# Kernel tuning notes

Measured on AMD Instinct MI355X. Metric: run time of the kernel, lower is better.

Reference implementation:

```python
import jax, jax.numpy as jnp
import numpy as np

NUM_BLOCKS = 4
B, S, D = 4, 4096, 1024
A, FF = 1024, 4096
LN_EPS = 1e-6


def _ln(x, s, b):
    m = jnp.mean(x, axis=-1, keepdims=True)
    v = jnp.mean(jnp.square(x - m), axis=-1, keepdims=True)
    return (x - m) * jax.lax.rsqrt(v + LN_EPS) * s + b


def setup_inputs() -> dict:
    key = jax.random.key(0)
    ks = jax.random.split(key, 8)
    w = lambda k, shape: jax.random.normal(k, shape, dtype=jnp.float32) * 0.02
    return {
        "x": jax.random.normal(ks[0], (B, S, D), dtype=jnp.float32),
        "Wq": w(ks[1], (NUM_BLOCKS, D, A)), "bq": jnp.zeros((NUM_BLOCKS, A), jnp.float32),
        "Wk": w(ks[2], (NUM_BLOCKS, D, A)), "bk": jnp.zeros((NUM_BLOCKS, A), jnp.float32),
        "Wv": w(ks[3], (NUM_BLOCKS, D, A)), "bv": jnp.zeros((NUM_BLOCKS, A), jnp.float32),
        "Wo": w(ks[4], (NUM_BLOCKS, A, D)), "bo": jnp.zeros((NUM_BLOCKS, D), jnp.float32),
        "ln1_s": jnp.ones((NUM_BLOCKS, D), jnp.float32), "ln1_b": jnp.zeros((NUM_BLOCKS, D), jnp.float32),
        "W1": w(ks[5], (NUM_BLOCKS, D, FF)), "b1": jnp.zeros((NUM_BLOCKS, FF), jnp.float32),
        "W2": w(ks[6], (NUM_BLOCKS, FF, D)), "b2": jnp.zeros((NUM_BLOCKS, D), jnp.float32),
        "ln2_s": jnp.ones((NUM_BLOCKS, D), jnp.float32), "ln2_b": jnp.zeros((NUM_BLOCKS, D), jnp.float32),
    }


def reference(x, Wq, bq, Wk, bk, Wv, bv, Wo, bo, ln1_s, ln1_b,
              W1, b1, W2, b2, ln2_s, ln2_b):
    for i in range(NUM_BLOCKS):
        residual = x
        # --- linear attention (elu+1 feature map, elementwise KV aggregation) ---
        q = x @ Wq[i] + bq[i]            # [B,S,A]
        k = x @ Wk[i] + bk[i]
        v = x @ Wv[i] + bv[i]
        Q = jax.nn.elu(q) + 1.0
        K = jax.nn.elu(k) + 1.0
        KV = jnp.einsum('nsh,nsh->nh', K, v, precision='highest')   # [B,A]
        Ksum = jnp.sum(K, axis=1)                                    # [B,A]
        Z = 1.0 / (Q * Ksum[:, None, :] + 1e-6)
        V = Q * KV[:, None, :] * Z                                   # [B,S,A]
        a = jax.nn.gelu(V @ Wo[i] + bo[i])   # gelu inside LinearAttention
        a = jax.nn.gelu(a)                   # gelu in the block body
        x = _ln(a + residual, ln1_s[i], ln1_b[i])
        # --- feedforward ---
        residual = x
        h = jax.nn.gelu(x @ W1[i] + b1[i])
        f = jax.nn.gelu(h @ W2[i] + b2[i])
        x = _ln(f + residual, ln2_s[i], ln2_b[i])
    return x
```

## Files before the change

### kernel.cpp

```cpp
#include <hip/hip_runtime.h>
#include <hip/hip_bf16.h>

typedef unsigned short u16;

#define B_  4
#define S_  4096
#define D_  1024
#define A_  1024
#define FF_ 4096
#define NB  4
#define LN_EPS 1e-6f

typedef __bf16 bf16x8 __attribute__((ext_vector_type(8)));
typedef float  floatx4 __attribute__((ext_vector_type(4)));

__device__ __forceinline__ float gelu_f(float x) {
    float u = 0.7978845608028654f * (x + 0.044715f * x * x * x);
    return x / (1.0f + __expf(-2.0f * u));
}

__device__ __forceinline__ u16 f2bf(float f) {
    __bf16 h = (__bf16)f;
    return *(u16*)&h;
}

__device__ __forceinline__ float bf2f(u16 u) {
    unsigned int v = ((unsigned int)u) << 16;
    float f;
    __builtin_memcpy(&f, &v, 4);
    return f;
}

__device__ __forceinline__ void gload_lds16(const u16* g, u16* l) {
    __builtin_amdgcn_global_load_lds(
        (const __attribute__((address_space(1))) void*)g,
        (__attribute__((address_space(3))) void*)l, 16, 0, 0);
}

__global__ __launch_bounds__(256) void zero_kv(float* __restrict__ p) {
    int idx = (blockIdx.x * 256 + threadIdx.x) * 4;
    *(float4*)(p + idx) = (float4){0.f, 0.f, 0.f, 0.f};
}

__global__ __launch_bounds__(256) void transpose_w(const float* __restrict__ W,
                                                   u16* __restrict__ Wt,
                                                   int K, int N) {
    __shared__ float tile[32][33];
    int tx = threadIdx.x;
    int ty = threadIdx.y;
    int n0 = blockIdx.x * 32;
    int k0 = blockIdx.y * 32;
#pragma unroll
    for (int r = 0; r < 4; r++) {
        int k = k0 + ty + r * 8;
        tile[ty + r * 8][tx] = W[(size_t)k * N + n0 + tx];
    }
    __syncthreads();
#pragma unroll
    for (int r = 0; r < 4; r++) {
        int n = n0 + ty + r * 8;
        Wt[(size_t)n * K + k0 + tx] = f2bf(tile[tx][ty + r * 8]);
    }
}

#define BAR  { asm volatile("" ::: "memory"); __builtin_amdgcn_s_barrier(); \
               asm volatile("" ::: "memory"); }
#define VMC4 asm volatile("s_waitcnt vmcnt(4)" ::: "memory")
#define PRIO1 __builtin_amdgcn_s_setprio(1)
#define PRIO0 __builtin_amdgcn_s_setprio(0)

#define STG(BASE, P, LD, BUF, H, KT) {                                         \
    const u16* s_ = (P) + (size_t)((H) * 128) * (LD) + (KT) * 64;              \
    u16* d_ = (BASE) + (BUF) * 16384 + (H) * 8192 + t * 8;                     \
    gload_lds16(s_, d_);                                                       \
    gload_lds16(s_ + (size_t)64 * (LD), d_ + 4096); }

#define LDA4(BUF, IH) {                                                        \
    _Pragma("unroll") for (int ii = 0; ii < 4; ii++) {                         \
        const u16* p_ = As0 + (BUF) * 16384 + aro + ((IH) * 4 + ii) * 1024;    \
        a[ii][0] = *(const bf16x8*)(p_ + sl0);                                 \
        a[ii][1] = *(const bf16x8*)(p_ + sl1); } }

#define LDB2(BUF, JH) {                                                        \
    _Pragma("unroll") for (int jj = 0; jj < 2; jj++) {                         \
        const u16* p_ = Bs0 + (BUF) * 16384 + bro + ((JH) * 2 + jj) * 1024;    \
        b[(JH) * 2 + jj][0] = *(const bf16x8*)(p_ + sl0);                      \
        b[(JH) * 2 + jj][1] = *(const bf16x8*)(p_ + sl1); } }

#define MM(IH, JH) {                                                           \
    _Pragma("unroll") for (int ii = 0; ii < 4; ii++)                           \
    _Pragma("unroll") for (int jj = 0; jj < 2; jj++)                           \
    _Pragma("unroll") for (int s = 0; s < 2; s++)                              \
        acc[(IH) * 4 + ii][(JH) * 2 + jj] =                                    \
            __builtin_amdgcn_mfma_f32_16x16x32_bf16(                           \
                a[ii][s], b[(JH) * 2 + jj][s],                                 \
                acc[(IH) * 4 + ii][(JH) * 2 + jj], 0, 0, 0); }

template <int MODE>
__global__ __launch_bounds__(512, 2) void gemm256(
    const u16* __restrict__ Amat, const u16* __restrict__ Bt,
    const float* __restrict__ bias, u16* __restrict__ out,
    int M, int N, int K, int gx, int ldo,
    u16* __restrict__ outK, u16* __restrict__ outV,
    const float* __restrict__ biasK, const float* __restrict__ biasV)
{
    __shared__ u16 shm[67584];
    u16* As0 = shm;
    u16* Bs0 = shm + 32768;

    const int nwg  = (int)gridDim.x;
    const int cpx  = nwg >> 3;
    const int wgid = ((int)blockIdx.x & 7) * cpx + ((int)blockIdx.x >> 3);
    const int bx = wgid % gx;
    const int by = wgid / gx;
    const int m0 = by * 256, n0 = bx * 256;

    const int t    = threadIdx.x;
    const int wid  = t >> 6, lane = t & 63;
    const int wm   = wid >> 2, wn = wid & 3;
    const int lm   = lane & 15, quad = lane >> 4;

    const int trow  = t >> 3;
    const int tslot = (t & 7) ^ (trow & 7);
    const u16* pa = Amat + (size_t)(m0 + trow) * K + tslot * 8;
    const u16* pb = Bt   + (size_t)(n0 + trow) * K + tslot * 8;

    const int aro = (wm * 128 + lm) * 64;
    const int bro = (wn * 64  + lm) * 64;
    const int sl0 = ((0 * 4 + quad) ^ (lm & 7)) * 8;
    const int sl1 = ((1 * 4 + quad) ^ (lm & 7)) * 8;

    floatx4 acc[8][4];
#pragma unroll
    for (int i = 0; i < 8; i++)
#pragma unroll
        for (int j = 0; j < 4; j++) acc[i][j] = (floatx4){0.f, 0.f, 0.f, 0.f};

    bf16x8 a[4][2], b[4][2];

    const int NT = K >> 6;
    const int NI = NT >> 1;

    STG(As0, pa, K, 0, 0, 0); STG(As0, pa, K, 0, 1, 0);
    STG(Bs0, pb, K, 0, 0, 0); STG(Bs0, pb, K, 0, 1, 0);
    STG(Bs0, pb, K, 1, 0, 1); STG(Bs0, pb, K, 1, 1, 1);
    VMC4; BAR;

    for (int it = 0; it < NI; it++) {
        const int T1 = 2 * it + 1;
        int T2 = 2 * it + 2; if (T2 > NT - 1) T2 = NT - 1;
        int T3 = 2 * it + 3; if (T3 > NT - 1) T3 = NT - 1;
        LDA4(0, 0); LDB2(0, 0);
        STG(As0, pa, K, 1, 0, T1);
        BAR; PRIO1; MM(0, 0); PRIO0; BAR;
        LDB2(0, 1);
        STG(As0, pa, K, 1, 1, T1);
        BAR; PRIO1; MM(0, 1); PRIO0; BAR;
        LDA4(0, 1);
        STG(Bs0, pb, K, 0, 0, T2);
        BAR; PRIO1; MM(1, 1); PRIO0; BAR;
        STG(Bs0, pb, K, 0, 1, T2);
        BAR; PRIO1; MM(1, 0); PRIO0; VMC4; BAR;
        LDA4(1, 0); LDB2(1, 0);
        STG(As0, pa, K, 0, 0, T2);
        BAR; PRIO1; MM(0, 0); PRIO0; BAR;
        LDB2(1, 1);
        STG(As0, pa, K, 0, 1, T2);
        BAR; PRIO1; MM(0, 1); PRIO0; BAR;
        LDA4(1, 1);
        STG(Bs0, pb, K, 1, 0, T3);
        BAR; PRIO1; MM(1, 1); PRIO0; BAR;
        STG(Bs0, pb, K, 1, 1, T3);
        BAR; PRIO1; MM(1, 0); PRIO0; VMC4; BAR;
    }

    asm volatile("s_waitcnt vmcnt(0)" ::: "memory");
    __syncthreads();

    const float* bp; u16* ob; int c0; bool elu;
    if (MODE == 4) {
        int seg = n0 >> 10;
        bp  = (seg == 0) ? bias : (seg == 1) ? biasK : biasV;
        ob  = (seg == 0) ? out  : (seg == 1) ? outK  : outV;
        c0  = n0 & 1023;
        elu = (seg < 2);
    } else { bp = bias; ob = out; c0 = n0; elu = false; }

    u16* Ct = shm;
#pragma unroll
    for (int j = 0; j < 4; j++) {
        int cl   = wn * 64 + j * 16 + lm;
        float bvl = bp[c0 + cl];
#pragma unroll
        for (int i = 0; i < 8; i++) {
            int rl = wm * 128 + i * 16 + quad * 4;
#pragma unroll
            for (int r = 0; r < 4; r++) {
                float z = acc[i][j][r] + bvl;
                float o;
                if (MODE == 2)      o = gelu_f(gelu_f(z));
                else if (MODE == 3) o = gelu_f(z);
                else if (MODE == 4) o = elu ? ((z > 0.f) ? z + 1.f : __expf(z)) : z;
                else                o = z;
                Ct[(rl + r) * 264 + cl] = f2bf(o);
            }
        }
    }
    __syncthreads();

    {
        int row = t >> 1;
        int ch  = (t & 1) * 128;
        const u16* src = Ct + row * 264 + ch;
        u16* dst = ob + (size_t)(m0 + row) * ldo + c0 + ch;
#pragma unroll
        for (int cc = 0; cc < 128; cc += 8)
            *(uint4*)(dst + cc) = *(const uint4*)(src + cc);
    }
}

__global__ __launch_bounds__(256) void kv_reduce(const u16* __restrict__ Kb,
                                                 const u16* __restrict__ vb,
                                                 float* __restrict__ KV,
                                                 float* __restrict__ Ks) {
    int n  = blockIdx.z;
    int h  = threadIdx.x * 4;
    int s0 = blockIdx.y * 128;
    const u16* kp = Kb + (size_t)n * S_ * A_ + (size_t)s0 * A_ + h;
    const u16* vp = vb + (size_t)n * S_ * A_ + (size_t)s0 * A_ + h;
    float kv0 = 0.f, kv1 = 0.f, kv2 = 0.f, kv3 = 0.f;
    float ks0 = 0.f, ks1 = 0.f, ks2 = 0.f, ks3 = 0.f;
#pragma unroll 4
    for (int s = 0; s < 128; s++) {
        ushort4 k4 = *(const ushort4*)(kp + (size_t)s * A_);
        ushort4 v4 = *(const ushort4*)(vp + (size_t)s * A_);
        float k0 = bf2f(k4.x), k1 = bf2f(k4.y), k2 = bf2f(k4.z), k3 = bf2f(k4.w);
        kv0 += k0 * bf2f(v4.x); kv1 += k1 * bf2f(v4.y);
        kv2 += k2 * bf2f(v4.z); kv3 += k3 * bf2f(v4.w);
        ks0 += k0; ks1 += k1; ks2 += k2; ks3 += k3;
    }
    int base = n * A_ + h;
    atomicAdd(&KV[base + 0], kv0); atomicAdd(&KV[base + 1], kv1);
    atomicAdd(&KV[base + 2], kv2); atomicAdd(&KV[base + 3], kv3);
    atomicAdd(&Ks[base + 0], ks0); atomicAdd(&Ks[base + 1], ks1);
    atomicAdd(&Ks[base + 2], ks2); atomicAdd(&Ks[base + 3], ks3);
}

__global__ __launch_bounds__(256) void linattn_ew(const u16* __restrict__ Qb,
                                                  const float* __restrict__ KV,
                                                  const float* __restrict__ Ks,
                                                  u16* __restrict__ vout) {
    size_t idx = ((size_t)blockIdx.x * 256 + threadIdx.x) * 4;
    int n = (int)(idx >> 22);
    int h = (int)(idx & (A_ - 1));
    ushort4 q4 = *(const ushort4*)(Qb + idx);
    int base = n * A_ + h;
    float4 kv4 = *(const float4*)(KV + base);
    float4 ks4 = *(const float4*)(Ks + base);
    float q0 = bf2f(q4.x), q1 = bf2f(q4.y), q2 = bf2f(q4.z), q3 = bf2f(q4.w);
    float o0 = q0 * kv4.x / (q0 * ks4.x + 1e-6f);
    float o1 = q1 * kv4.y / (q1 * ks4.y + 1e-6f);
    float o2 = q2 * kv4.z / (q2 * ks4.z + 1e-6f);
    float o3 = q3 * kv4.w / (q3 * ks4.w + 1e-6f);
    ushort4 o;
    o.x = f2bf(o0); o.y = f2bf(o1); o.z = f2bf(o2); o.w = f2bf(o3);
    *(ushort4*)(vout + idx) = o;
}

__global__ __launch_bounds__(256) void convert_x(const float* __restrict__ x,
                                                 float* __restrict__ xf,
                                                 u16* __restrict__ xb) {
    size_t idx = ((size_t)blockIdx.x * 256 + threadIdx.x) * 4;
    float4 v = *(const float4*)(x + idx);
    *(float4*)(xf + idx) = v;
    ushort4 o;
    o.x = f2bf(v.x); o.y = f2bf(v.y); o.z = f2bf(v.z); o.w = f2bf(v.w);
    *(ushort4*)(xb + idx) = o;
}

__global__ __launch_bounds__(256) void ln_fused(const u16* y,
                                                const float* res,
                                                const float* sc,
                                                const float* bs,
                                                float* xf,
                                                u16* xb) {
    __shared__ float wred[8];
    int row = blockIdx.x;
    int t   = threadIdx.x;
    int lane = t & 63, wid = t >> 6;
    const u16*   yp = y   + (size_t)row * D_;
    const float* rp = res + (size_t)row * D_;
    ushort4 y4 = *(const ushort4*)(yp + t * 4);
    float4  r4 = *(const float4*)(rp + t * 4);
    float v0 = bf2f(y4.x) + r4.x;
    float v1 = bf2f(y4.y) + r4.y;
    float v2 = bf2f(y4.z) + r4.z;
    float v3 = bf2f(y4.w) + r4.w;
    float s = v0 + v1 + v2 + v3;
#pragma unroll
    for (int o = 32; o; o >>= 1) s += __shfl_down(s, o, 64);
    if (lane == 0) wred[wid] = s;
    __syncthreads();
    float mean = (wred[0] + wred[1] + wred[2] + wred[3]) * (1.0f / D_);
    float d0 = v0 - mean, d1 = v1 - mean, d2 = v2 - mean, d3 = v3 - mean;
    float q = d0 * d0 + d1 * d1 + d2 * d2 + d3 * d3;
#pragma unroll
    for (int o = 32; o; o >>= 1) q += __shfl_down(q, o, 64);
    if (lane == 0) wred[wid + 4] = q;
    __syncthreads();
    float rstd = rsqrtf((wred[4] + wred[5] + wred[6] + wred[7]) * (1.0f / D_) + LN_EPS);
    float4 s4 = *(const float4*)(sc + t * 4);
    float4 b4 = *(const float4*)(bs + t * 4);
    float o0 = d0 * rstd * s4.x + b4.x;
    float o1 = d1 * rstd * s4.y + b4.y;
    float o2 = d2 * rstd * s4.z + b4.z;
    float o3 = d3 * rstd * s4.w + b4.w;
    *(float4*)(xf + (size_t)row * D_ + t * 4) = (float4){o0, o1, o2, o3};
    ushort4 ob;
    ob.x = f2bf(o0); ob.y = f2bf(o1); ob.z = f2bf(o2); ob.w = f2bf(o3);
    *(ushort4*)(xb + (size_t)row * D_ + t * 4) = ob;
}

extern "C" void kernel_launch(void* const* d_in, const int* in_sizes, int n_in,
                              void* d_out, int out_size, void* d_ws, size_t ws_size,
                              hipStream_t stream) {
    const float* x_in = (const float*)d_in[0];
    const float* Wq   = (const float*)d_in[1];
    const float* bq   = (const float*)d_in[2];
    const float* Wk   = (const float*)d_in[3];
    const float* bk   = (const float*)d_in[4];
    const float* Wv   = (const float*)d_in[5];
    const float* bv   = (const float*)d_in[6];
    const float* Wo   = (const float*)d_in[7];
    const float* bo   = (const float*)d_in[8];
    const float* ln1s = (const float*)d_in[9];
    const float* ln1b = (const float*)d_in[10];
    const float* W1   = (const float*)d_in[11];
    const float* b1   = (const float*)d_in[12];
    const float* W2   = (const float*)d_in[13];
    const float* b2   = (const float*)d_in[14];
    const float* ln2s = (const float*)d_in[15];
    const float* ln2b = (const float*)d_in[16];

    const size_t MB = 1024 * 1024;
    char* ws = (char*)d_ws;
    float* xf    = (float*)d_out;
    u16*   xb    = (u16*)(ws);
    u16*   Qb    = (u16*)(ws + 32 * MB);
    u16*   Kb    = (u16*)(ws + 64 * MB);
    u16*   vb    = (u16*)(ws + 96 * MB);
    u16*   hid   = (u16*)(ws + 32 * MB);
    u16*   WtQKV = (u16*)(ws + 128 * MB);
    u16*   Wot   = (u16*)(ws + 134 * MB);
    float* kvb   = (float*)(ws + 136 * MB);
    u16*   W1t   = (u16*)(ws + 160 * MB);
    u16*   W2t   = (u16*)(ws + 168 * MB);
    float* KV    = kvb;
    float* Ks    = kvb + B_ * A_;

    const int M = B_ * S_;

    convert_x<<<dim3(M * D_ / 1024), 256, 0, stream>>>(x_in, xf, xb);

    for (int i = 0; i < NB; i++) {
        const float* Wq_i = Wq + (size_t)i * D_ * A_;
        const float* Wk_i = Wk + (size_t)i * D_ * A_;
        const float* Wv_i = Wv + (size_t)i * D_ * A_;
        const float* Wo_i = Wo + (size_t)i * A_ * D_;
        const float* W1_i = W1 + (size_t)i * D_ * FF_;
        const float* W2_i = W2 + (size_t)i * FF_ * D_;

        transpose_w<<<dim3(A_ / 32, D_ / 32), dim3(32, 8), 0, stream>>>(Wq_i, WtQKV, D_, A_);
        transpose_w<<<dim3(A_ / 32, D_ / 32), dim3(32, 8), 0, stream>>>(Wk_i, WtQKV + (size_t)A_ * D_, D_, A_);
        transpose_w<<<dim3(A_ / 32, D_ / 32), dim3(32, 8), 0, stream>>>(Wv_i, WtQKV + (size_t)2 * A_ * D_, D_, A_);
        transpose_w<<<dim3(D_ / 32, A_ / 32), dim3(32, 8), 0, stream>>>(Wo_i, Wot, A_, D_);
        transpose_w<<<dim3(FF_ / 32, D_ / 32), dim3(32, 8), 0, stream>>>(W1_i, W1t, D_, FF_);
        transpose_w<<<dim3(D_ / 32, FF_ / 32), dim3(32, 8), 0, stream>>>(W2_i, W2t, FF_, D_);

        gemm256<4><<<dim3(12 * 64), 512, 0, stream>>>(
            xb, WtQKV, bq + i * A_, Qb, M, 3072, D_, 12, 1024,
            Kb, vb, bk + i * A_, bv + i * A_);

        zero_kv<<<dim3(8), 256, 0, stream>>>(kvb);
        kv_reduce<<<dim3(1, S_ / 128, B_), 256, 0, stream>>>(Kb, vb, KV, Ks);

        linattn_ew<<<dim3(M * A_ / 1024), 256, 0, stream>>>(Qb, KV, Ks, Kb);

        gemm256<2><<<dim3(4 * 64), 512, 0, stream>>>(
            Kb, Wot, bo + i * D_, vb, M, D_, A_, 4, 1024,
            nullptr, nullptr, nullptr, nullptr);

        ln_fused<<<dim3(M), 256, 0, stream>>>(vb, xf, ln1s + i * D_, ln1b + i * D_, xf, xb);

        gemm256<3><<<dim3(16 * 64), 512, 0, stream>>>(
            xb, W1t, b1 + (size_t)i * FF_, hid, M, FF_, D_, 16, 4096,
            nullptr, nullptr, nullptr, nullptr);
        gemm256<3><<<dim3(4 * 64), 512, 0, stream>>>(
            hid, W2t, b2 + i * D_, xb, M, D_, FF_, 4, 1024,
            nullptr, nullptr, nullptr, nullptr);

        ln_fused<<<dim3(M), 256, 0, stream>>>(xb, xf, ln2s + i * D_, ln2b + i * D_, xf, xb);
    }
}
```

Measured before the change: 2.677 ms.

## Restructure GEMM main loop with triple-buffered B and register double-buffered A fragments

```diff
diff --git a/kernel.cpp b/kernel.cpp
--- a/kernel.cpp
+++ b/kernel.cpp
@@ -65,36 +65,34 @@
 
 #define BAR  { asm volatile("" ::: "memory"); __builtin_amdgcn_s_barrier(); \
                asm volatile("" ::: "memory"); }
-#define VMC4 asm volatile("s_waitcnt vmcnt(4)" ::: "memory")
+#define VMC(N) asm volatile("s_waitcnt vmcnt(" #N ")" ::: "memory")
 #define PRIO1 __builtin_amdgcn_s_setprio(1)
 #define PRIO0 __builtin_amdgcn_s_setprio(0)
 
-#define STG(BASE, P, LD, BUF, H, KT) {                                         \
+#define STG(OFF, P, LD, H, KT) {                                               \
     const u16* s_ = (P) + (size_t)((H) * 128) * (LD) + (KT) * 64;              \
-    u16* d_ = (BASE) + (BUF) * 16384 + (H) * 8192 + t * 8;                     \
+    u16* d_ = shm + (OFF) + (H) * 8192 + t * 8;                                \
     gload_lds16(s_, d_);                                                       \
     gload_lds16(s_ + (size_t)64 * (LD), d_ + 4096); }
 
-#define LDA4(BUF, IH) {                                                        \
-    _Pragma("unroll") for (int ii = 0; ii < 4; ii++) {                         \
-        const u16* p_ = As0 + (BUF) * 16384 + aro + ((IH) * 4 + ii) * 1024;    \
-        a[ii][0] = *(const bf16x8*)(p_ + sl0);                                 \
-        a[ii][1] = *(const bf16x8*)(p_ + sl1); } }
-
-#define LDB2(BUF, JH) {                                                        \
-    _Pragma("unroll") for (int jj = 0; jj < 2; jj++) {                         \
-        const u16* p_ = Bs0 + (BUF) * 16384 + bro + ((JH) * 2 + jj) * 1024;    \
-        b[(JH) * 2 + jj][0] = *(const bf16x8*)(p_ + sl0);                      \
-        b[(JH) * 2 + jj][1] = *(const bf16x8*)(p_ + sl1); } }
-
-#define MM(IH, JH) {                                                           \
-    _Pragma("unroll") for (int ii = 0; ii < 4; ii++)                           \
-    _Pragma("unroll") for (int jj = 0; jj < 2; jj++)                           \
+#define LDA2(AOFF, PAIR, SL) {                                                 \
+    _Pragma("unroll") for (int ii = 0; ii < 2; ii++) {                         \
+        const u16* p_ = shm + (AOFF) + aro + ((PAIR) * 2 + ii) * 1024;         \
+        a[SL][ii][0] = *(const bf16x8*)(p_ + sl0);                             \
+        a[SL][ii][1] = *(const bf16x8*)(p_ + sl1); } }
+
+#define LDBALL(BOFF) {                                                         \
+    _Pragma("unroll") for (int jj = 0; jj < 4; jj++) {                         \
+        const u16* p_ = shm + (BOFF) + bro + jj * 1024;                        \
+        b[jj][0] = *(const bf16x8*)(p_ + sl0);                                 \
+        b[jj][1] = *(const bf16x8*)(p_ + sl1); } }
+
+#define MMC(SL, C) {                                                           \
+    _Pragma("unroll") for (int ii = 0; ii < 2; ii++)                           \
+    _Pragma("unroll") for (int jj = 0; jj < 4; jj++)                           \
     _Pragma("unroll") for (int s = 0; s < 2; s++)                              \
-        acc[(IH) * 4 + ii][(JH) * 2 + jj] =                                    \
-            __builtin_amdgcn_mfma_f32_16x16x32_bf16(                           \
-                a[ii][s], b[(JH) * 2 + jj][s],                                 \
-                acc[(IH) * 4 + ii][(JH) * 2 + jj], 0, 0, 0); }
+        acc[(C) * 2 + ii][jj] = __builtin_amdgcn_mfma_f32_16x16x32_bf16(       \
+            a[SL][ii][s], b[jj][s], acc[(C) * 2 + ii][jj], 0, 0, 0); }
 
 template <int MODE>
 __global__ __launch_bounds__(512, 2) void gemm256(
@@ -104,9 +102,7 @@
     u16* __restrict__ outK, u16* __restrict__ outV,
     const float* __restrict__ biasK, const float* __restrict__ biasV)
 {
-    __shared__ u16 shm[67584];
-    u16* As0 = shm;
-    u16* Bs0 = shm + 32768;
+    __shared__ u16 shm[81920];
 
     const int nwg  = (int)gridDim.x;
     const int cpx  = nwg >> 3;
@@ -136,42 +132,43 @@
 #pragma unroll
         for (int j = 0; j < 4; j++) acc[i][j] = (floatx4){0.f, 0.f, 0.f, 0.f};
 
-    bf16x8 a[4][2], b[4][2];
+    bf16x8 a[2][2][2];
+    bf16x8 b[4][2];
+
+    int aCur = 0,      aNxt = 16384;
+    int bCur = 32768,  bNx1 = 49152, bNx2 = 65536;
 
     const int NT = K >> 6;
-    const int NI = NT >> 1;
-
-    STG(As0, pa, K, 0, 0, 0); STG(As0, pa, K, 0, 1, 0);
-    STG(Bs0, pb, K, 0, 0, 0); STG(Bs0, pb, K, 0, 1, 0);
-    STG(Bs0, pb, K, 1, 0, 1); STG(Bs0, pb, K, 1, 1, 1);
-    VMC4; BAR;
-
-    for (int it = 0; it < NI; it++) {
-        const int T1 = 2 * it + 1;
-        int T2 = 2 * it + 2; if (T2 > NT - 1) T2 = NT - 1;
-        int T3 = 2 * it + 3; if (T3 > NT - 1) T3 = NT - 1;
-        LDA4(0, 0); LDB2(0, 0);
-        STG(As0, pa, K, 1, 0, T1);
-        BAR; PRIO1; MM(0, 0); PRIO0; BAR;
-        LDB2(0, 1);
-        STG(As0, pa, K, 1, 1, T1);
-        BAR; PRIO1; MM(0, 1); PRIO0; BAR;
-        LDA4(0, 1);
-        STG(Bs0, pb, K, 0, 0, T2);
-        BAR; PRIO1; MM(1, 1); PRIO0; BAR;
-        STG(Bs0, pb, K, 0, 1, T2);
-        BAR; PRIO1; MM(1, 0); PRIO0; VMC4; BAR;
-        LDA4(1, 0); LDB2(1, 0);
-        STG(As0, pa, K, 0, 0, T2);
-        BAR; PRIO1; MM(0, 0); PRIO0; BAR;
-        LDB2(1, 1);
-        STG(As0, pa, K, 0, 1, T2);
-        BAR; PRIO1; MM(0, 1); PRIO0; BAR;
-        LDA4(1, 1);
-        STG(Bs0, pb, K, 1, 0, T3);
-        BAR; PRIO1; MM(1, 1); PRIO0; BAR;
-        STG(Bs0, pb, K, 1, 1, T3);
-        BAR; PRIO1; MM(1, 0); PRIO0; VMC4; BAR;
+
+    STG(aCur, pa, K, 0, 0); STG(aCur, pa, K, 1, 0);
+    STG(bCur, pb, K, 0, 0); STG(bCur, pb, K, 1, 0);
+    STG(bNx1, pb, K, 0, 1); STG(bNx1, pb, K, 1, 1);
+    VMC(4);
+    BAR;
+    LDBALL(bCur);
+    LDA2(aCur, 0, 0);
+
+    for (int tt = 0; tt < NT; tt++) {
+        int t1 = tt + 1; if (t1 > NT - 1) t1 = NT - 1;
+        int t2 = tt + 2; if (t2 > NT - 1) t2 = NT - 1;
+        LDA2(aCur, 1, 1);
+        STG(aNxt, pa, K, 0, t1);
+        BAR; PRIO1; MMC(0, 0); PRIO0; BAR;
+        LDA2(aCur, 2, 0);
+        STG(aNxt, pa, K, 1, t1);
+        BAR; PRIO1; MMC(1, 1); PRIO0; BAR;
+        LDA2(aCur, 3, 1);
+        STG(bNx2, pb, K, 0, t2);
+        BAR; PRIO1; MMC(0, 2); PRIO0;
+        VMC(2);
+        BAR;
+        STG(bNx2, pb, K, 1, t2);
+        BAR; PRIO1; MMC(1, 3); PRIO0;
+        LDBALL(bNx1);
+        LDA2(aNxt, 0, 0);
+        BAR;
+        int tmp = aCur; aCur = aNxt; aNxt = tmp;
+        tmp = bCur; bCur = bNx1; bNx1 = bNx2; bNx2 = tmp;
     }
 
     asm volatile("s_waitcnt vmcnt(0)" ::: "memory");
```

Measured after the change: 2.606 ms. -2.6%, faster.

## Make GEMM persistent with cross-tile prefetch and staged epilogue

Applied to the files above, without the earlier changes.

```diff
diff --git a/kernel.cpp b/kernel.cpp
--- a/kernel.cpp
+++ b/kernel.cpp
@@ -65,25 +65,26 @@
 
 #define BAR  { asm volatile("" ::: "memory"); __builtin_amdgcn_s_barrier(); \
                asm volatile("" ::: "memory"); }
-#define VMC4 asm volatile("s_waitcnt vmcnt(4)" ::: "memory")
+#define LBAR { asm volatile("s_waitcnt lgkmcnt(0)" ::: "memory"); BAR; }
+#define VMC(N) asm volatile("s_waitcnt vmcnt(" #N ")" ::: "memory")
 #define PRIO1 __builtin_amdgcn_s_setprio(1)
 #define PRIO0 __builtin_amdgcn_s_setprio(0)
 
-#define STG(BASE, P, LD, BUF, H, KT) {                                         \
-    const u16* s_ = (P) + (size_t)((H) * 128) * (LD) + (KT) * 64;              \
-    u16* d_ = (BASE) + (BUF) * 16384 + (H) * 8192 + t * 8;                     \
+#define STG(OFF, P, H, KT) {                                                   \
+    const u16* s_ = (P) + (size_t)((H) * 128) * K + (KT) * 64;                 \
+    u16* d_ = shm + (OFF) + (H) * 8192 + t * 8;                                \
     gload_lds16(s_, d_);                                                       \
-    gload_lds16(s_ + (size_t)64 * (LD), d_ + 4096); }
+    gload_lds16(s_ + (size_t)64 * K, d_ + 4096); }
 
 #define LDA4(BUF, IH) {                                                        \
     _Pragma("unroll") for (int ii = 0; ii < 4; ii++) {                         \
-        const u16* p_ = As0 + (BUF) * 16384 + aro + ((IH) * 4 + ii) * 1024;    \
+        const u16* p_ = shm + (BUF) * 16384 + aro + ((IH) * 4 + ii) * 1024;    \
         a[ii][0] = *(const bf16x8*)(p_ + sl0);                                 \
         a[ii][1] = *(const bf16x8*)(p_ + sl1); } }
 
 #define LDB2(BUF, JH) {                                                        \
     _Pragma("unroll") for (int jj = 0; jj < 2; jj++) {                         \
-        const u16* p_ = Bs0 + (BUF) * 16384 + bro + ((JH) * 2 + jj) * 1024;    \
+        const u16* p_ = shm + 32768 + (BUF) * 16384 + bro + ((JH)*2+jj)*1024;  \
         b[(JH) * 2 + jj][0] = *(const bf16x8*)(p_ + sl0);                      \
         b[(JH) * 2 + jj][1] = *(const bf16x8*)(p_ + sl1); } }
 
@@ -97,23 +98,18 @@
                 acc[(IH) * 4 + ii][(JH) * 2 + jj], 0, 0, 0); }
 
 template <int MODE>
-__global__ __launch_bounds__(512, 2) void gemm256(
+__global__ __launch_bounds__(512, 2) void gemm256p(
     const u16* __restrict__ Amat, const u16* __restrict__ Bt,
     const float* __restrict__ bias, u16* __restrict__ out,
-    int M, int N, int K, int gx, int ldo,
+    int K, int gx, int ntiles, int ldo,
     u16* __restrict__ outK, u16* __restrict__ outV,
     const float* __restrict__ biasK, const float* __restrict__ biasV)
 {
-    __shared__ u16 shm[67584];
-    u16* As0 = shm;
-    u16* Bs0 = shm + 32768;
-
-    const int nwg  = (int)gridDim.x;
-    const int cpx  = nwg >> 3;
-    const int wgid = ((int)blockIdx.x & 7) * cpx + ((int)blockIdx.x >> 3);
-    const int bx = wgid % gx;
-    const int by = wgid / gx;
-    const int m0 = by * 256, n0 = bx * 256;
+    __shared__ u16 shm[81920];
+    u16* Es = shm + 65536;
+
+    const int wgid = ((int)blockIdx.x & 7) * 32 + ((int)blockIdx.x >> 3);
+    const int tpb  = ntiles >> 8;
 
     const int t    = threadIdx.x;
     const int wid  = t >> 6, lane = t & 63;
@@ -122,101 +118,131 @@
 
     const int trow  = t >> 3;
     const int tslot = (t & 7) ^ (trow & 7);
-    const u16* pa = Amat + (size_t)(m0 + trow) * K + tslot * 8;
-    const u16* pb = Bt   + (size_t)(n0 + trow) * K + tslot * 8;
 
     const int aro = (wm * 128 + lm) * 64;
     const int bro = (wn * 64  + lm) * 64;
     const int sl0 = ((0 * 4 + quad) ^ (lm & 7)) * 8;
     const int sl1 = ((1 * 4 + quad) ^ (lm & 7)) * 8;
 
-    floatx4 acc[8][4];
-#pragma unroll
-    for (int i = 0; i < 8; i++)
-#pragma unroll
-        for (int j = 0; j < 4; j++) acc[i][j] = (floatx4){0.f, 0.f, 0.f, 0.f};
-
-    bf16x8 a[4][2], b[4][2];
-
     const int NT = K >> 6;
     const int NI = NT >> 1;
 
-    STG(As0, pa, K, 0, 0, 0); STG(As0, pa, K, 0, 1, 0);
-    STG(Bs0, pb, K, 0, 0, 0); STG(Bs0, pb, K, 0, 1, 0);
-    STG(Bs0, pb, K, 1, 0, 1); STG(Bs0, pb, K, 1, 1, 1);
-    VMC4; BAR;
-
-    for (int it = 0; it < NI; it++) {
-        const int T1 = 2 * it + 1;
-        int T2 = 2 * it + 2; if (T2 > NT - 1) T2 = NT - 1;
-        int T3 = 2 * it + 3; if (T3 > NT - 1) T3 = NT - 1;
-        LDA4(0, 0); LDB2(0, 0);
-        STG(As0, pa, K, 1, 0, T1);
-        BAR; PRIO1; MM(0, 0); PRIO0; BAR;
-        LDB2(0, 1);
-        STG(As0, pa, K, 1, 1, T1);
-        BAR; PRIO1; MM(0, 1); PRIO0; BAR;
-        LDA4(0, 1);
-        STG(Bs0, pb, K, 0, 0, T2);
-        BAR; PRIO1; MM(1, 1); PRIO0; BAR;
-        STG(Bs0, pb, K, 0, 1, T2);
-        BAR; PRIO1; MM(1, 0); PRIO0; VMC4; BAR;
-        LDA4(1, 0); LDB2(1, 0);
-        STG(As0, pa, K, 0, 0, T2);
-        BAR; PRIO1; MM(0, 0); PRIO0; BAR;
-        LDB2(1, 1);
-        STG(As0, pa, K, 0, 1, T2);
-        BAR; PRIO1; MM(0, 1); PRIO0; BAR;
-        LDA4(1, 1);
-        STG(Bs0, pb, K, 1, 0, T3);
-        BAR; PRIO1; MM(1, 1); PRIO0; BAR;
-        STG(Bs0, pb, K, 1, 1, T3);
-        BAR; PRIO1; MM(1, 0); PRIO0; VMC4; BAR;
-    }
-
-    asm volatile("s_waitcnt vmcnt(0)" ::: "memory");
-    __syncthreads();
-
-    const float* bp; u16* ob; int c0; bool elu;
-    if (MODE == 4) {
-        int seg = n0 >> 10;
-        bp  = (seg == 0) ? bias : (seg == 1) ? biasK : biasV;
-        ob  = (seg == 0) ? out  : (seg == 1) ? outK  : outV;
-        c0  = n0 & 1023;
-        elu = (seg < 2);
-    } else { bp = bias; ob = out; c0 = n0; elu = false; }
-
-    u16* Ct = shm;
-#pragma unroll
-    for (int j = 0; j < 4; j++) {
-        int cl   = wn * 64 + j * 16 + lm;
-        float bvl = bp[c0 + cl];
-#pragma unroll
-        for (int i = 0; i < 8; i++) {
-            int rl = wm * 128 + i * 16 + quad * 4;
-#pragma unroll
-            for (int r = 0; r < 4; r++) {
-                float z = acc[i][j][r] + bvl;
-                float o;
-                if (MODE == 2)      o = gelu_f(gelu_f(z));
-                else if (MODE == 3) o = gelu_f(z);
-                else if (MODE == 4) o = elu ? ((z > 0.f) ? z + 1.f : __expf(z)) : z;
-                else                o = z;
-                Ct[(rl + r) * 264 + cl] = f2bf(o);
+    floatx4 acc[8][4];
+    bf16x8 a[4][2], b[4][2];
+
+    int id0 = wgid * tpb;
+    int bx = id0 % gx, by = id0 / gx;
+
+    {
+        const u16* pa = Amat + (size_t)(by * 256 + trow) * K + tslot * 8;
+        const u16* pb = Bt   + (size_t)(bx * 256 + trow) * K + tslot * 8;
+        STG(0,     pa, 0, 0); STG(0,     pa, 1, 0);
+        STG(32768, pb, 0, 0); STG(32768, pb, 1, 0);
+        STG(49152, pb, 0, 1); STG(49152, pb, 1, 1);
+    }
+
+    for (int tl = 0; tl < tpb; tl++) {
+        int nbx = bx, nby = by;
+        if (tl < tpb - 1) { nbx = bx + 1; if (nbx == gx) { nbx = 0; nby = by + 1; } }
+        const int m0 = by * 256, n0 = bx * 256;
+        const u16* pa  = Amat + (size_t)(m0 + trow) * K + tslot * 8;
+        const u16* pb  = Bt   + (size_t)(n0 + trow) * K + tslot * 8;
+        const u16* pa2 = Amat + (size_t)(nby * 256 + trow) * K + tslot * 8;
+        const u16* pb2 = Bt   + (size_t)(nbx * 256 + trow) * K + tslot * 8;
+
+        const float* bp; u16* ob; int c0; bool elu;
+        if (MODE == 4) {
+            int seg = n0 >> 10;
+            bp  = (seg == 0) ? bias : (seg == 1) ? biasK : biasV;
+            ob  = (seg == 0) ? out  : (seg == 1) ? outK  : outV;
+            c0  = n0 & 1023;
+            elu = (seg < 2);
+        } else { bp = bias; ob = out; c0 = n0; elu = false; }
+
+        VMC(4); BAR;
+
+        float bvl[4];
+#pragma unroll
+        for (int j = 0; j < 4; j++) bvl[j] = bp[c0 + wn * 64 + j * 16 + lm];
+
+#pragma unroll
+        for (int i = 0; i < 8; i++)
+#pragma unroll
+            for (int j = 0; j < 4; j++) acc[i][j] = (floatx4){0.f, 0.f, 0.f, 0.f};
+
+        for (int it = 0; it < NI; it++) {
+            const int T1 = 2 * it + 1;
+            const bool lst = (it == NI - 1);
+            const u16* qa = lst ? pa2 : pa;
+            const u16* qb = lst ? pb2 : pb;
+            const int  k2 = lst ? 0 : 2 * it + 2;
+            const int  k3 = lst ? 1 : 2 * it + 3;
+            LDA4(0, 0); LDB2(0, 0);
+            STG(16384, pa, 0, T1);
+            BAR; PRIO1; MM(0, 0); PRIO0; BAR;
+            LDB2(0, 1);
+            STG(16384, pa, 1, T1);
+            BAR; PRIO1; MM(0, 1); PRIO0; BAR;
+            LDA4(0, 1);
+            STG(32768, qb, 0, k2);
+            BAR; PRIO1; MM(1, 1); PRIO0; BAR;
+            STG(32768, qb, 1, k2);
+            BAR; PRIO1; MM(1, 0); PRIO0; VMC(4); BAR;
+            LDA4(1, 0); LDB2(1, 0);
+            STG(0, qa, 0, k2);
+            BAR; PRIO1; MM(0, 0); PRIO0; BAR;
+            LDB2(1, 1);
+            STG(0, qa, 1, k2);
+            BAR; PRIO1; MM(0, 1); PRIO0; BAR;
+            LDA4(1, 1);
+            STG(49152, qb, 0, k3);
+            BAR; PRIO1; MM(1, 1); PRIO0; BAR;
+            STG(49152, qb, 1, k3);
+            BAR; PRIO1; MM(1, 0); PRIO0; VMC(4); BAR;
+        }
+
+#pragma unroll
+        for (int p = 0; p < 4; p++) {
+            if (wm == (p >> 1)) {
+                const int ibase = 4 * (p & 1);
+#pragma unroll
+                for (int j = 0; j < 4; j++) {
+                    int cl = wn * 64 + j * 16 + lm;
+                    int slot = cl >> 3, off = cl & 7;
+#pragma unroll
+                    for (int i2 = 0; i2 < 4; i2++) {
+#pragma unroll
+                        for (int r = 0; r < 4; r++) {
+                            float z = acc[ibase + i2][j][r] + bvl[j];
+                            float o;
+                            if (MODE == 2)      o = gelu_f(gelu_f(z));
+                            else if (MODE == 3) o = gelu_f(z);
+                            else if (MODE == 4) o = elu ? ((z > 0.f) ? z + 1.f : __expf(z)) : z;
+                            else                o = z;
+                            int rloc = i2 * 16 + quad * 4 + r;
+                            Es[rloc * 256 + ((slot ^ (quad << 2)) * 8) + off] = f2bf(o);
+                        }
+                    }
+                }
             }
+            LBAR;
+            {
+                int rl = t >> 3;
+                int g  = t & 7;
+                u16* dst = ob + (size_t)(m0 + p * 64 + rl) * ldo + c0 + g * 32;
+#pragma unroll
+                for (int k = 0; k < 4; k++) {
+                    int slot = g * 4 + k;
+                    uint4 v = *(const uint4*)(Es + rl * 256 + ((slot ^ (rl & 12)) * 8));
+                    *(uint4*)(dst + k * 8) = v;
+                }
+            }
+            BAR;
         }
-    }
-    __syncthreads();
-
-    {
-        int row = t >> 1;
-        int ch  = (t & 1) * 128;
-        const u16* src = Ct + row * 264 + ch;
-        u16* dst = ob + (size_t)(m0 + row) * ldo + c0 + ch;
-#pragma unroll
-        for (int cc = 0; cc < 128; cc += 8)
-            *(uint4*)(dst + cc) = *(const uint4*)(src + cc);
-    }
+
+        bx = nbx; by = nby;
+    }
+    VMC(0);
 }
 
 __global__ __launch_bounds__(256) void kv_reduce(const u16* __restrict__ Kb,
@@ -377,8 +403,8 @@
         transpose_w<<<dim3(FF_ / 32, D_ / 32), dim3(32, 8), 0, stream>>>(W1_i, W1t, D_, FF_);
         transpose_w<<<dim3(D_ / 32, FF_ / 32), dim3(32, 8), 0, stream>>>(W2_i, W2t, FF_, D_);
 
-        gemm256<4><<<dim3(12 * 64), 512, 0, stream>>>(
-            xb, WtQKV, bq + i * A_, Qb, M, 3072, D_, 12, 1024,
+        gemm256p<4><<<dim3(256), 512, 0, stream>>>(
+            xb, WtQKV, bq + i * A_, Qb, D_, 12, 768, 1024,
             Kb, vb, bk + i * A_, bv + i * A_);
 
         zero_kv<<<dim3(8), 256, 0, stream>>>(kvb);
@@ -386,17 +412,17 @@
 
         linattn_ew<<<dim3(M * A_ / 1024), 256, 0, stream>>>(Qb, KV, Ks, Kb);
 
-        gemm256<2><<<dim3(4 * 64), 512, 0, stream>>>(
-            Kb, Wot, bo + i * D_, vb, M, D_, A_, 4, 1024,
+        gemm256p<2><<<dim3(256), 512, 0, stream>>>(
+            Kb, Wot, bo + i * D_, vb, A_, 4, 256, 1024,
             nullptr, nullptr, nullptr, nullptr);
 
         ln_fused<<<dim3(M), 256, 0, stream>>>(vb, xf, ln1s + i * D_, ln1b + i * D_, xf, xb);
 
-        gemm256<3><<<dim3(16 * 64), 512, 0, stream>>>(
-            xb, W1t, b1 + (size_t)i * FF_, hid, M, FF_, D_, 16, 4096,
+        gemm256p<3><<<dim3(256), 512, 0, stream>>>(
+            xb, W1t, b1 + (size_t)i * FF_, hid, D_, 16, 1024, 4096,
             nullptr, nullptr, nullptr, nullptr);
-        gemm256<3><<<dim3(4 * 64), 512, 0, stream>>>(
-            hid, W2t, b2 + i * D_, xb, M, D_, FF_, 4, 1024,
+        gemm256p<3><<<dim3(256), 512, 0, stream>>>(
+            hid, W2t, b2 + i * D_, xb, FF_, 4, 256, 1024,
             nullptr, nullptr, nullptr, nullptr);
 
         ln_fused<<<dim3(M), 256, 0, stream>>>(xb, xf, ln2s + i * D_, ln2b + i * D_, xf, xb);
```

New measurement: 2.708 ms. About the same (+1.2%).

## Triple-buffer B tiles in LDS and drop redundant barriers in GEMM loop

Applied to the files above, without the earlier changes.

```diff
diff --git a/kernel.cpp b/kernel.cpp
--- a/kernel.cpp
+++ b/kernel.cpp
@@ -65,25 +65,25 @@
 
 #define BAR  { asm volatile("" ::: "memory"); __builtin_amdgcn_s_barrier(); \
                asm volatile("" ::: "memory"); }
-#define VMC4 asm volatile("s_waitcnt vmcnt(4)" ::: "memory")
+#define VMC(N) asm volatile("s_waitcnt vmcnt(" #N ")" ::: "memory")
 #define PRIO1 __builtin_amdgcn_s_setprio(1)
 #define PRIO0 __builtin_amdgcn_s_setprio(0)
 
-#define STG(BASE, P, LD, BUF, H, KT) {                                         \
-    const u16* s_ = (P) + (size_t)((H) * 128) * (LD) + (KT) * 64;              \
-    u16* d_ = (BASE) + (BUF) * 16384 + (H) * 8192 + t * 8;                     \
+#define STG(OFF, P, H, KT) {                                                   \
+    const u16* s_ = (P) + (size_t)((H) * 128) * K + (KT) * 64;                 \
+    u16* d_ = shm + (OFF) + (H) * 8192 + t * 8;                                \
     gload_lds16(s_, d_);                                                       \
-    gload_lds16(s_ + (size_t)64 * (LD), d_ + 4096); }
-
-#define LDA4(BUF, IH) {                                                        \
+    gload_lds16(s_ + (size_t)64 * K, d_ + 4096); }
+
+#define LDA4(OFF, IH) {                                                        \
     _Pragma("unroll") for (int ii = 0; ii < 4; ii++) {                         \
-        const u16* p_ = As0 + (BUF) * 16384 + aro + ((IH) * 4 + ii) * 1024;    \
+        const u16* p_ = shm + (OFF) + aro + ((IH) * 4 + ii) * 1024;            \
         a[ii][0] = *(const bf16x8*)(p_ + sl0);                                 \
         a[ii][1] = *(const bf16x8*)(p_ + sl1); } }
 
-#define LDB2(BUF, JH) {                                                        \
+#define LDB2(OFF, JH) {                                                        \
     _Pragma("unroll") for (int jj = 0; jj < 2; jj++) {                         \
-        const u16* p_ = Bs0 + (BUF) * 16384 + bro + ((JH) * 2 + jj) * 1024;    \
+        const u16* p_ = shm + (OFF) + bro + ((JH) * 2 + jj) * 1024;            \
         b[(JH) * 2 + jj][0] = *(const bf16x8*)(p_ + sl0);                      \
         b[(JH) * 2 + jj][1] = *(const bf16x8*)(p_ + sl1); } }
 
@@ -104,9 +104,7 @@
     u16* __restrict__ outK, u16* __restrict__ outV,
     const float* __restrict__ biasK, const float* __restrict__ biasV)
 {
-    __shared__ u16 shm[67584];
-    u16* As0 = shm;
-    u16* Bs0 = shm + 32768;
+    __shared__ u16 shm[81920];
 
     const int nwg  = (int)gridDim.x;
     const int cpx  = nwg >> 3;
@@ -139,39 +137,32 @@
     bf16x8 a[4][2], b[4][2];
 
     const int NT = K >> 6;
-    const int NI = NT >> 1;
-
-    STG(As0, pa, K, 0, 0, 0); STG(As0, pa, K, 0, 1, 0);
-    STG(Bs0, pb, K, 0, 0, 0); STG(Bs0, pb, K, 0, 1, 0);
-    STG(Bs0, pb, K, 1, 0, 1); STG(Bs0, pb, K, 1, 1, 1);
-    VMC4; BAR;
-
-    for (int it = 0; it < NI; it++) {
-        const int T1 = 2 * it + 1;
-        int T2 = 2 * it + 2; if (T2 > NT - 1) T2 = NT - 1;
-        int T3 = 2 * it + 3; if (T3 > NT - 1) T3 = NT - 1;
-        LDA4(0, 0); LDB2(0, 0);
-        STG(As0, pa, K, 1, 0, T1);
-        BAR; PRIO1; MM(0, 0); PRIO0; BAR;
-        LDB2(0, 1);
-        STG(As0, pa, K, 1, 1, T1);
-        BAR; PRIO1; MM(0, 1); PRIO0; BAR;
-        LDA4(0, 1);
-        STG(Bs0, pb, K, 0, 0, T2);
-        BAR; PRIO1; MM(1, 1); PRIO0; BAR;
-        STG(Bs0, pb, K, 0, 1, T2);
-        BAR; PRIO1; MM(1, 0); PRIO0; VMC4; BAR;
-        LDA4(1, 0); LDB2(1, 0);
-        STG(As0, pa, K, 0, 0, T2);
-        BAR; PRIO1; MM(0, 0); PRIO0; BAR;
-        LDB2(1, 1);
-        STG(As0, pa, K, 0, 1, T2);
-        BAR; PRIO1; MM(0, 1); PRIO0; BAR;
-        LDA4(1, 1);
-        STG(Bs0, pb, K, 1, 0, T3);
-        BAR; PRIO1; MM(1, 1); PRIO0; BAR;
-        STG(Bs0, pb, K, 1, 1, T3);
-        BAR; PRIO1; MM(1, 0); PRIO0; VMC4; BAR;
+
+    STG(0,     pa, 0, 0); STG(0,     pa, 1, 0);
+    STG(32768, pb, 0, 0); STG(32768, pb, 1, 0);
+    STG(49152, pb, 0, 1); STG(49152, pb, 1, 1);
+    VMC(4); BAR;
+
+    int aCur = 0,     aNxt = 16384;
+    int bB0 = 32768,  bB1 = 49152, bB2 = 65536;
+
+    for (int tt = 0; tt < NT; tt++) {
+        int t1 = tt + 1; if (t1 > NT - 1) t1 = NT - 1;
+        int t2 = tt + 2; if (t2 > NT - 1) t2 = NT - 1;
+        LDA4(aCur, 0); LDB2(bB0, 0);
+        STG(aNxt, pa, 0, t1);
+        BAR; PRIO1; MM(0, 0); PRIO0;
+        LDB2(bB0, 1);
+        STG(aNxt, pa, 1, t1);
+        BAR; PRIO1; MM(0, 1); PRIO0;
+        LDA4(aCur, 1);
+        STG(bB2, pb, 0, t2);
+        BAR; PRIO1; MM(1, 1); PRIO0;
+        STG(bB2, pb, 1, t2);
+        VMC(4);
+        BAR; PRIO1; MM(1, 0); PRIO0;
+        int tmp = aCur; aCur = aNxt; aNxt = tmp;
+        tmp = bB0; bB0 = bB1; bB1 = bB2; bB2 = tmp;
     }
 
     asm volatile("s_waitcnt vmcnt(0)" ::: "memory");
```

Measured after the change: 2.682 ms. Within noise of the previous version (+0.2%).
